# Optimization experiments

Hardware: AMD Instinct MI355X
Metric: run time of the kernel (lower is better)

Reference implementation:

```python
import jax, jax.numpy as jnp
import numpy as np

B, SQ, SKV = 4, 2048, 2048
DQ, DKV, H, NH = 1024, 1024, 1024, 16
HD = H // NH


def setup_inputs() -> dict:
    key = jax.random.key(0)
    ks = jax.random.split(key, 10)
    s = 0.02
    return {
        "query": jax.random.normal(ks[0], (B, SQ, DQ), jnp.float32),
        "key_value": jax.random.normal(ks[1], (B, SKV, DKV), jnp.float32),
        "Wq": jax.random.normal(ks[2], (DQ, H), jnp.float32) * s,
        "bq": jnp.zeros((H,), jnp.float32),
        "Wk": jax.random.normal(ks[3], (DKV, H), jnp.float32) * s,
        "bk": jnp.zeros((H,), jnp.float32),
        "Wv": jax.random.normal(ks[4], (DKV, H), jnp.float32) * s,
        "bv": jnp.zeros((H,), jnp.float32),
        "Wo": jax.random.normal(ks[5], (H, DQ), jnp.float32) * s,
        "bo": jnp.zeros((DQ,), jnp.float32),
    }


def reference(query, key_value, Wq, bq, Wk, bk, Wv, bv, Wo, bo):
    b, sq, _ = query.shape
    skv = key_value.shape[1]
    scale = np.sqrt(HD).astype(np.float32)
    # project and split heads: [B, S, H] -> [B, NH, S, HD]
    q = (query @ Wq + bq).reshape(b, sq, NH, HD).transpose(0, 2, 1, 3)
    k = (key_value @ Wk + bk).reshape(b, skv, NH, HD).transpose(0, 2, 1, 3)
    v = (key_value @ Wv + bv).reshape(b, skv, NH, HD).transpose(0, 2, 1, 3)
    scores = jnp.einsum("bhqd,bhkd->bhqk", q, k) / scale
    attn = jax.nn.softmax(scores, axis=-1)
    out = jnp.einsum("bhqk,bhkd->bhqd", attn, v)
    out = out.transpose(0, 2, 1, 3).reshape(b, sq, NH * HD)
    return out @ Wo + bo
```

## Files before the change

kernel.cpp:

```cpp
#include <hip/hip_runtime.h>


typedef short s16x8 __attribute__((ext_vector_type(8)));
typedef short s16x4 __attribute__((ext_vector_type(4)));
typedef float f32x4 __attribute__((ext_vector_type(4)));
typedef float f32x16 __attribute__((ext_vector_type(16)));
typedef unsigned short u16;
typedef unsigned int u32;

__device__ __forceinline__ u16 f2bf(float f){
    union{float f;u32 u;} v; v.f=f;
    u32 r = v.u + 0x7fffu + ((v.u>>16)&1u);
    return (u16)(r>>16);
}
__device__ __forceinline__ int swz(int row,int colB){ return row*128 + (colB ^ ((row&7)<<4)); }

__device__ __forceinline__ void gl16(const void* g, void* l){
    __builtin_amdgcn_global_load_lds((__attribute__((address_space(1))) void*)(void*)g,
                                     (__attribute__((address_space(3))) void*)l, 16, 0, 0);
}
__device__ __forceinline__ u32 cvtpk(float lo, float hi){
    u32 r; asm("v_cvt_pk_bf16_f32 %0, %1, %2" : "=v"(r) : "v"(lo), "v"(hi)); return r;
}
__device__ __forceinline__ void plswap(u32& a, u32& b){
    asm("v_permlane32_swap_b32 %0, %1" : "+v"(a), "+v"(b));
}

#define QSCALE 0.1803368801111204f

__device__ __forceinline__ void transW_body(const float* __restrict__ W, u16* __restrict__ Wt,
                                            int n0, int k0){
    __shared__ u16 T[64*68];
    const int tid = threadIdx.x;
    const int tr = tid>>4, tc = (tid&15)*4;
    #pragma unroll
    for (int p=0;p<4;++p){
        int k = p*16 + tr;
        f32x4 v = *(const f32x4*)(W + (size_t)(k0+k)*1024 + n0 + tc);
        s16x4 o;
        #pragma unroll
        for (int j=0;j<4;++j) o[j]=(short)f2bf(v[j]);
        *(s16x4*)(T + k*68 + tc) = o;
    }
    __syncthreads();
    #pragma unroll
    for (int p=0;p<4;++p){
        int n = p*16 + tr;
        s16x4 o;
        #pragma unroll
        for (int e=0;e<4;++e) o[e] = (short)T[(tc+e)*68 + n];
        *(s16x4*)(Wt + (size_t)(n0+n)*1024 + k0 + tc) = o;
    }
}

__global__ __launch_bounds__(256)
void prep(const float* __restrict__ q, const float* __restrict__ kv,
          u16* __restrict__ qbf, u16* __restrict__ kvbf,
          const float* __restrict__ W0, const float* __restrict__ W1,
          const float* __restrict__ W2, const float* __restrict__ W3,
          u16* __restrict__ T0, u16* __restrict__ T1,
          u16* __restrict__ T2, u16* __restrict__ T3)
{
    int blk = blockIdx.x;
    if (blk < 8192){
        const float* in = q; u16* out = qbf;
        if (blk >= 4096){ in = kv; out = kvbf; blk -= 4096; }
        size_t i = ((size_t)blk*256 + threadIdx.x)*8;
        f32x4 x = *(const f32x4*)(in+i), y = *(const f32x4*)(in+i+4);
        s16x8 o;
        #pragma unroll
        for (int j=0;j<4;++j){ o[j]=(short)f2bf(x[j]); o[4+j]=(short)f2bf(y[j]); }
        *(s16x8*)(out+i) = o;
    } else {
        blk -= 8192;
        int w = blk>>8, rem = blk&255;
        const float* W = (w==0)?W0:(w==1)?W1:(w==2)?W2:W3;
        u16*      Wt  = (w==0)?T0:(w==1)?T1:(w==2)?T2:T3;
        transW_body(W, Wt, (rem&15)*64, (rem>>4)*64);
    }
}

__global__ __launch_bounds__(256)
void gemm_qkv(const u16* __restrict__ qbf, const u16* __restrict__ kvbf,
              const u16* __restrict__ Wt3,
              const float* __restrict__ bq, const float* __restrict__ bk,
              const float* __restrict__ bv,
              u16* __restrict__ Qb, u16* __restrict__ Kb, u16* __restrict__ Vtb)
{
    __shared__ __align__(16) u16 As[2][128*64];
    __shared__ __align__(16) u16 Bs[2][128*64];
    const int K = 1024, N = 1024;
    const int tid = threadIdx.x, lane = tid&63, wave = tid>>6;
    const int ln = lane&15, g = lane>>4;
    const int wm = wave>>1, wn = wave&1;
    const int bm = blockIdx.x;
    const int proj = blockIdx.y >> 3, bn = blockIdx.y & 7;

    const u16* A    = proj ? kvbf : qbf;
    const u16* Bt   = Wt3 + (size_t)proj*(1024*1024);
    const float* bias = (proj==0) ? bq : (proj==1 ? bk : bv);
    const float scale = (proj==0) ? QSCALE : 1.0f;

    f32x4 acc[4][4] = {};

    const int r0g = tid>>3, cc8 = (tid&7)*8;
    const u16* aA = A  + (size_t)(bm*128 + r0g)*K + cc8;
    const u16* aB = Bt + (size_t)(bn*128 + r0g)*K + cc8;

    auto stage = [&](int k0, int buf){
        char* pa = (char*)As[buf] + tid*16;
        char* pb = (char*)Bs[buf] + tid*16;
        #pragma unroll
        for (int i=0;i<4;++i){
            gl16(aA + k0 + i*32*K, pa + i*4096);
            gl16(aB + k0 + i*32*K, pb + i*4096);
        }
    };

    stage(0, 0);
    int cur = 0;
    for (int k0=0; k0<K; k0+=64){
        if (k0+64 < K){
            stage(k0+64, cur^1);
            asm volatile("s_waitcnt vmcnt(8)" ::: "memory");
        } else {
            asm volatile("s_waitcnt vmcnt(0)" ::: "memory");
        }
        __builtin_amdgcn_s_barrier();
        #pragma unroll
        for (int kk=0;kk<2;++kk){
            s16x8 af[4], bf[4];
            #pragma unroll
            for (int mi=0;mi<4;++mi)
                af[mi] = *(const s16x8*)((const char*)As[cur] + (size_t)(wm*64+mi*16+ln)*128 + kk*64 + g*16);
            #pragma unroll
            for (int ni=0;ni<4;++ni)
                bf[ni] = *(const s16x8*)((const char*)Bs[cur] + (size_t)(wn*64+ni*16+ln)*128 + kk*64 + g*16);
            #pragma unroll
            for (int mi=0;mi<4;++mi)
                #pragma unroll
                for (int ni=0;ni<4;++ni)
                    acc[mi][ni] = __builtin_amdgcn_mfma_f32_16x16x32_bf16(af[mi], bf[ni], acc[mi][ni], 0,0,0);
        }
        __builtin_amdgcn_s_barrier();
        cur ^= 1;
    }

    if (proj == 2){
        u16* T = (u16*)As;
        #pragma unroll
        for (int mi=0;mi<4;++mi){
            #pragma unroll
            for (int ni=0;ni<4;++ni){
                int colp = wn*64 + ni*16 + ln;
                int row0 = wm*64 + mi*16 + 4*g;
                float bvv = bias[bn*128 + colp];
                s16x4 pk4;
                #pragma unroll
                for (int r=0;r<4;++r) pk4[r] = (short)f2bf(acc[mi][ni][r] + bvv);
                *(s16x4*)((char*)T + colp*256 + ((row0*2) ^ ((colp&7)<<4))) = pk4;
            }
        }
        __syncthreads();
        const int cold = tid>>1, chunk = (tid&1)*64;
        const int b = bm>>4, sbase = (bm*128)&2047;
        u16* dst = Vtb + ((size_t)(b*1024 + bn*128 + cold))*2048 + sbase + chunk;
        #pragma unroll
        for (int i=0;i<8;++i){
            s16x8 vv = *(const s16x8*)((char*)T + cold*256 + (((chunk + i*8)*2) ^ ((cold&7)<<4)));
            *(s16x8*)(dst + i*8) = vv;
        }
    } else {
        u16* C = proj ? Kb : Qb;
        #pragma unroll
        for (int mi=0;mi<4;++mi){
            #pragma unroll
            for (int ni=0;ni<4;++ni){
                int col = bn*128 + wn*64 + ni*16 + ln;
                float bvv = bias[col];
                #pragma unroll
                for (int r=0;r<4;++r){
                    int row = bm*128 + wm*64 + mi*16 + 4*g + r;
                    C[(size_t)row*N + col] = f2bf((acc[mi][ni][r] + bvv) * scale);
                }
            }
        }
    }
}

__global__ __launch_bounds__(256)
void gemm_out(const u16* __restrict__ A, const u16* __restrict__ Bt,
              const float* __restrict__ bias, float* __restrict__ C,
              int M, int N, int K)
{
    __shared__ __align__(16) u16 As[2][128*64];
    __shared__ __align__(16) u16 Bs[2][128*64];
    const int tid = threadIdx.x, lane = tid&63, wave = tid>>6;
    const int ln = lane&15, g = lane>>4;
    const int wm = wave>>1, wn = wave&1;
    const int bm = blockIdx.x, bn = blockIdx.y;

    f32x4 acc[4][4] = {};

    const int r0g = tid>>3, cc8 = (tid&7)*8;
    const u16* aA = A  + (size_t)(bm*128 + r0g)*K + cc8;
    const u16* aB = Bt + (size_t)(bn*128 + r0g)*K + cc8;

    auto stage = [&](int k0, int buf){
        char* pa = (char*)As[buf] + tid*16;
        char* pb = (char*)Bs[buf] + tid*16;
        #pragma unroll
        for (int i=0;i<4;++i){
            gl16(aA + k0 + i*32*K, pa + i*4096);
            gl16(aB + k0 + i*32*K, pb + i*4096);
        }
    };

    stage(0, 0);
    int cur = 0;
    for (int k0=0; k0<K; k0+=64){
        if (k0+64 < K){
            stage(k0+64, cur^1);
            asm volatile("s_waitcnt vmcnt(8)" ::: "memory");
        } else {
            asm volatile("s_waitcnt vmcnt(0)" ::: "memory");
        }
        __builtin_amdgcn_s_barrier();
        #pragma unroll
        for (int kk=0;kk<2;++kk){
            s16x8 af[4], bf[4];
            #pragma unroll
            for (int mi=0;mi<4;++mi)
                af[mi] = *(const s16x8*)((const char*)As[cur] + (size_t)(wm*64+mi*16+ln)*128 + kk*64 + g*16);
            #pragma unroll
            for (int ni=0;ni<4;++ni)
                bf[ni] = *(const s16x8*)((const char*)Bs[cur] + (size_t)(wn*64+ni*16+ln)*128 + kk*64 + g*16);
            #pragma unroll
            for (int mi=0;mi<4;++mi)
                #pragma unroll
                for (int ni=0;ni<4;++ni)
                    acc[mi][ni] = __builtin_amdgcn_mfma_f32_16x16x32_bf16(af[mi], bf[ni], acc[mi][ni], 0,0,0);
        }
        __builtin_amdgcn_s_barrier();
        cur ^= 1;
    }

    #pragma unroll
    for (int mi=0;mi<4;++mi){
        #pragma unroll
        for (int ni=0;ni<4;++ni){
            int col = bn*128 + wn*64 + ni*16 + ln;
            float bv = bias[col];
            #pragma unroll
            for (int r=0;r<4;++r){
                int row = bm*128 + wm*64 + mi*16 + 4*g + r;
                C[(size_t)row*N + col] = acc[mi][ni][r] + bv;
            }
        }
    }
}

__global__ __launch_bounds__(256)
void attn_fwd13(const u16* __restrict__ Q, const u16* __restrict__ K,
                const u16* __restrict__ Vt, u16* __restrict__ O)
{
    __shared__ __align__(16) char smem[32768];
    const int tid = threadIdx.x, lane = tid&63, wave = tid>>6;
    const int l31 = lane&31, hl = lane>>5;

    int dlin = blockIdx.y*16 + blockIdx.x;
    int xc = dlin&7, t0 = dlin>>3;
    int bh = xc*8 + (t0>>4), qt = t0&15;
    int b = bh>>4, h = bh&15;

    const int qrow = qt*128 + wave*32 + l31;
    const size_t qgoff = ((size_t)(b*2048 + qrow))*1024 + h*64;
    const u16* Kg = K  + ((size_t)(b*2048))*1024 + h*64;
    const u16* Vg = Vt + ((size_t)(b*1024 + h*64))*2048;

    s16x8 bq[4];
    #pragma unroll
    for (int ks=0;ks<4;++ks)
        bq[ks] = *(const s16x8*)(Q + qgoff + 16*ks + 8*hl);

    float lacc[8] = {};
    f32x16 oa0 = {}, oa1 = {};

    const int r0 = tid>>3;
    const int qc = (tid&7) ^ (r0&7);
    const u16* kbase = Kg + (size_t)r0*1024 + qc*8;
    const u16* vbase = Vg + (size_t)r0*2048 + qc*8;
    const int ldst = tid*16;

    auto stage = [&](int kt, int buf){
        char* Kb = smem + buf*16384;
        char* Vb = Kb + 8192;
        const size_t kkOff = (size_t)kt*65536;
        const int kv0 = kt*64;
        gl16(kbase + kkOff,           Kb + ldst);
        gl16(kbase + kkOff + 32768,   Kb + 4096 + ldst);
        gl16(vbase + kv0,             Vb + ldst);
        gl16(vbase + kv0 + 65536,     Vb + 4096 + ldst);
    };

    int kofs[8];
    #pragma unroll
    for (int hk=0;hk<2;++hk)
        #pragma unroll
        for (int ks=0;ks<4;++ks)
            kofs[hk*4+ks] = swz(hk*32 + l31, 32*ks + 16*hl);

    auto qk = [&](int buf, f32x16& sA, f32x16& sB){
        char* Kb = smem + buf*16384;
        f32x16 a = {}, c = {};
        __builtin_amdgcn_s_setprio(1);
        #pragma unroll
        for (int ks=0; ks<4; ++ks){
            s16x8 ak0 = *(const s16x8*)(Kb + kofs[ks]);
            s16x8 ak1 = *(const s16x8*)(Kb + kofs[4+ks]);
            a = __builtin_amdgcn_mfma_f32_32x32x16_bf16(ak0, bq[ks], a, 0,0,0);
            c = __builtin_amdgcn_mfma_f32_32x32x16_bf16(ak1, bq[ks], c, 0,0,0);
        }
        __builtin_amdgcn_s_setprio(0);
        sA = a; sB = c;
    };

    auto smpack = [&](f32x16& s0, f32x16& s1, s16x8* bP){
        #pragma unroll
        for (int r=0; r<16; ++r){
            s0[r] = __builtin_amdgcn_exp2f(s0[r]);
            s1[r] = __builtin_amdgcn_exp2f(s1[r]);
        }
        #pragma unroll
        for (int i=0;i<8;++i)
            lacc[i] += (s0[i]+s0[i+8]) + (s1[i]+s1[i+8]);
        #pragma unroll
        for (int f=0; f<2; ++f){
            const f32x16& sf = f ? s1 : s0;
            u32 W[8];
            #pragma unroll
            for (int w=0; w<8; ++w) W[w] = cvtpk(sf[2*w], sf[2*w+1]);
            #pragma unroll
            for (int s=0; s<2; ++s){
                u32 x0 = W[4*s+0], y0 = W[4*s+2];
                u32 x1 = W[4*s+1], y1 = W[4*s+3];
                plswap(x0, y0);
                plswap(x1, y1);
                union { u32 w[4]; s16x8 v; } u;
                u.w[0]=x0; u.w[1]=x1; u.w[2]=y0; u.w[3]=y1;
                bP[2*f+s] = u.v;
            }
        }
    };

    auto pv = [&](int buf, const s16x8* bP){
        char* Vb = smem + buf*16384 + 8192;
        __builtin_amdgcn_s_setprio(1);
        #pragma unroll
        for (int ks=0; ks<4; ++ks){
            s16x8 av0 = *(const s16x8*)(Vb + kofs[ks]);
            s16x8 av1 = *(const s16x8*)(Vb + kofs[4+ks]);
            oa0 = __builtin_amdgcn_mfma_f32_32x32x16_bf16(av0, bP[ks], oa0, 0,0,0);
            oa1 = __builtin_amdgcn_mfma_f32_32x32x16_bf16(av1, bP[ks], oa1, 0,0,0);
        }
        __builtin_amdgcn_s_setprio(0);
    };

    int cur = 0;
    auto body = [&](f32x16& sC0, f32x16& sC1, f32x16& sN0, f32x16& sN1, int kt){
        asm volatile("s_waitcnt vmcnt(2)" ::: "memory");
        __builtin_amdgcn_s_barrier();
        qk(cur^1, sN0, sN1);
        s16x8 bP[4];
        smpack(sC0, sC1, bP);
        pv(cur, bP);
        __builtin_amdgcn_s_barrier();
        if (kt < 30) stage(kt+2, cur);
        cur ^= 1;
    };

    stage(0, 0);
    stage(1, 1);
    asm volatile("s_waitcnt vmcnt(6)" ::: "memory");
    __builtin_amdgcn_s_barrier();
    f32x16 sa, sb, sc, sd;
    qk(0, sa, sb);

    int kt = 0;
    #pragma unroll 1
    for (int it=0; it<15; ++it){
        body(sa, sb, sc, sd, kt); ++kt;
        body(sc, sd, sa, sb, kt); ++kt;
    }
    body(sa, sb, sc, sd, kt); ++kt;

    asm volatile("s_waitcnt vmcnt(0)" ::: "memory");
    __builtin_amdgcn_s_barrier();
    {
        s16x8 bP[4];
        smpack(sc, sd, bP);
        pv(cur, bP);
    }

    float rs = ((lacc[0]+lacc[1])+(lacc[2]+lacc[3])) + ((lacc[4]+lacc[5])+(lacc[6]+lacc[7]));
    rs += __shfl_xor(rs, 32);
    float inv = 1.0f / rs;

    u16* Ob = O + qgoff;
    #pragma unroll
    for (int fd=0; fd<2; ++fd){
        const f32x16& oaf = fd ? oa1 : oa0;
        #pragma unroll
        for (int rq=0; rq<4; ++rq){
            s16x4 o;
            #pragma unroll
            for (int e=0;e<4;++e) o[e] = (short)f2bf(oaf[rq*4+e] * inv);
            *(s16x4*)(Ob + fd*32 + rq*8 + hl*4) = o;
        }
    }
}

template<bool A_IS_F32, int EPI>
__global__ __launch_bounds__(256)
void gemm_bias_64(const void* __restrict__ Av, const float* __restrict__ W,
                  const float* __restrict__ bias, void* __restrict__ Cout,
                  int M, int N, int K, float scale)
{
    __shared__ __align__(16) char smem[16384];
    char* As = smem;
    char* Ws = smem + 8192;
    const int tid  = threadIdx.x;
    const int lane = tid & 63, wave = tid >> 6;
    const int g = lane >> 4, ln = lane & 15;
    const int wm = wave >> 1, wn = wave & 1;
    const int bm = blockIdx.x, bn = blockIdx.y;
    f32x4 acc[2][2] = {};
    const int srow = tid >> 2;
    const int sch  = (tid & 3) * 16;

    for (int k0 = 0; k0 < K; k0 += 64) {
        if constexpr (A_IS_F32) {
            const float* a = (const float*)Av + (size_t)(bm*64+srow)*K + k0 + sch;
            const f32x4* a4 = (const f32x4*)a;
            #pragma unroll
            for (int c = 0; c < 2; ++c) {
                f32x4 x = a4[c*2+0], y = a4[c*2+1];
                s16x8 wv;
                #pragma unroll
                for (int j = 0; j < 4; ++j){ wv[j]=(short)f2bf(x[j]); wv[4+j]=(short)f2bf(y[j]); }
                *(s16x8*)(As + swz(srow, sch*2 + c*16)) = wv;
            }
        } else {
            const u16* a = (const u16*)Av + (size_t)(bm*64+srow)*K + k0 + sch;
            *(s16x8*)(As + swz(srow, sch*2 + 0))  = *(const s16x8*)(a + 0);
            *(s16x8*)(As + swz(srow, sch*2 + 16)) = *(const s16x8*)(a + 8);
        }
        {
            const float* wsrc = W + (size_t)(k0+srow)*N + bn*64 + sch;
            #pragma unroll
            for (int j = 0; j < 16; ++j) {
                int n = sch + j;
                *(short*)(Ws + n*128 + ((srow*2) ^ ((n&7)<<4))) = (short)f2bf(wsrc[j]);
            }
        }
        __syncthreads();
        #pragma unroll
        for (int kk = 0; kk < 2; ++kk) {
            s16x8 af[2], bfr[2];
            #pragma unroll
            for (int mi = 0; mi < 2; ++mi)
                af[mi] = *(const s16x8*)(As + swz(wm*32+mi*16+ln, kk*64 + g*16));
            #pragma unroll
            for (int ni = 0; ni < 2; ++ni)
                bfr[ni] = *(const s16x8*)(Ws + swz(wn*32+ni*16+ln, kk*64 + g*16));
            #pragma unroll
            for (int mi = 0; mi < 2; ++mi)
                #pragma unroll
                for (int ni = 0; ni < 2; ++ni)
                    acc[mi][ni] = __builtin_amdgcn_mfma_f32_16x16x32_bf16(af[mi], bfr[ni], acc[mi][ni], 0,0,0);
        }
        __syncthreads();
    }
    #pragma unroll
    for (int mi = 0; mi < 2; ++mi){
        #pragma unroll
        for (int ni = 0; ni < 2; ++ni){
            int col = bn*64 + wn*32 + ni*16 + ln;
            float bv = bias[col];
            #pragma unroll
            for (int r = 0; r < 4; ++r){
                int row = bm*64 + wm*32 + mi*16 + 4*g + r;
                float v = (acc[mi][ni][r] + bv) * scale;
                if constexpr (EPI==0)
                    ((u16*)Cout)[(size_t)row*N + col] = f2bf(v);
                else if constexpr (EPI==2){
                    int b = row>>11, s = row&2047;
                    ((u16*)Cout)[((size_t)(b*1024+col))*2048 + s] = f2bf(v);
                } else
                    ((float*)Cout)[(size_t)row*N + col] = v;
            }
        }
    }
}

extern "C" void kernel_launch(void* const* d_in, const int* in_sizes, int n_in,
                              void* d_out, int out_size, void* d_ws, size_t ws_size,
                              hipStream_t stream)
{
    const float* query = (const float*)d_in[0];
    const float* kvin  = (const float*)d_in[1];
    const float* Wq = (const float*)d_in[2];
    const float* bq = (const float*)d_in[3];
    const float* Wk = (const float*)d_in[4];
    const float* bk = (const float*)d_in[5];
    const float* Wv = (const float*)d_in[6];
    const float* bv = (const float*)d_in[7];
    const float* Wo = (const float*)d_in[8];
    const float* bo = (const float*)d_in[9];

    const int M = 8192, D = 1024;
    const size_t MB = 1024ull*1024ull;
    u16* Qb  = (u16*)d_ws;
    u16* Kb  = Qb  + 8*MB;
    u16* Vtb = Kb  + 8*MB;
    u16* Ob  = Vtb + 8*MB;

    if (ws_size >= 66*MB) {
        u16* Wt3 = Ob;
        u16* Wto = Ob + 8*MB;
        u16* qbf  = (u16*)d_out;
        u16* kvbf = qbf + 8*MB;

        prep<<<9216,256,0,stream>>>(query, kvin, qbf, kvbf,
                                    Wq, Wk, Wv, Wo,
                                    Wt3, Wt3 + 1*MB, Wt3 + 2*MB, Wto);

        gemm_qkv<<<dim3(64,24),256,0,stream>>>(qbf, kvbf, Wt3, bq, bk, bv,
                                               Qb, Kb, Vtb);

        attn_fwd13<<<dim3(16,64),256,0,stream>>>(Qb, Kb, Vtb, Ob);

        gemm_out<<<dim3(64,8),256,0,stream>>>(Ob, Wto, bo, (float*)d_out, M, D, D);
    } else {
        dim3 gg(128,16);
        gemm_bias_64<true ,0><<<gg,256,0,stream>>>(query, Wq, bq, Qb,  M, D, D, QSCALE);
        gemm_bias_64<true ,0><<<gg,256,0,stream>>>(kvin,  Wk, bk, Kb,  M, D, D, 1.0f);
        gemm_bias_64<true ,2><<<gg,256,0,stream>>>(kvin,  Wv, bv, Vtb, M, D, D, 1.0f);
        attn_fwd13<<<dim3(16,64),256,0,stream>>>(Qb, Kb, Vtb, Ob);
        gemm_bias_64<false,3><<<gg,256,0,stream>>>(Ob, Wo, bo, d_out, M, D, D, 1.0f);
    }
}
```

Baseline: 216.7 us.

## Fuse Q projection into attention kernel and drop Q from QKV GEMM

The Q projection leaves the batched QKV GEMM, which now computes only K and V. Each attention block instead computes its own 128×64 Q tile with MFMA from bf16 query rows and transposed Wq loaded straight from global memory, then adds bias, scales and packs it into the B-operand layout. This removes the Q write and re-read and one third of the projection GEMM grid, and the first K/V tiles are staged before the Q compute to overlap that latency. In exchange, Q-projection loads bypass LDS, so each wave fetches the same Wq slice redundantly with strided global loads, which adds latency and L2 traffic at the start of attention.

```diff
diff --git a/kernel.cpp b/kernel.cpp
--- a/kernel.cpp
+++ b/kernel.cpp
@@ -81,11 +81,9 @@
 }
 
 __global__ __launch_bounds__(256)
-void gemm_qkv(const u16* __restrict__ qbf, const u16* __restrict__ kvbf,
-              const u16* __restrict__ Wt3,
-              const float* __restrict__ bq, const float* __restrict__ bk,
-              const float* __restrict__ bv,
-              u16* __restrict__ Qb, u16* __restrict__ Kb, u16* __restrict__ Vtb)
+void gemm_kv(const u16* __restrict__ kvbf, const u16* __restrict__ WtKV,
+             const float* __restrict__ bk, const float* __restrict__ bv,
+             u16* __restrict__ Kb, u16* __restrict__ Vtb)
 {
     __shared__ __align__(16) u16 As[2][128*64];
     __shared__ __align__(16) u16 Bs[2][128*64];
@@ -96,16 +94,14 @@
     const int bm = blockIdx.x;
     const int proj = blockIdx.y >> 3, bn = blockIdx.y & 7;
 
-    const u16* A    = proj ? kvbf : qbf;
-    const u16* Bt   = Wt3 + (size_t)proj*(1024*1024);
-    const float* bias = (proj==0) ? bq : (proj==1 ? bk : bv);
-    const float scale = (proj==0) ? QSCALE : 1.0f;
+    const u16* Bt   = WtKV + (size_t)proj*(1024*1024);
+    const float* bias = proj ? bv : bk;
 
     f32x4 acc[4][4] = {};
 
     const int r0g = tid>>3, cc8 = (tid&7)*8;
-    const u16* aA = A  + (size_t)(bm*128 + r0g)*K + cc8;
-    const u16* aB = Bt + (size_t)(bn*128 + r0g)*K + cc8;
+    const u16* aA = kvbf + (size_t)(bm*128 + r0g)*K + cc8;
+    const u16* aB = Bt   + (size_t)(bn*128 + r0g)*K + cc8;
 
     auto stage = [&](int k0, int buf){
         char* pa = (char*)As[buf] + tid*16;
@@ -146,7 +142,7 @@
         cur ^= 1;
     }
 
-    if (proj == 2){
+    if (proj == 1){
         u16* T = (u16*)As;
         #pragma unroll
         for (int mi=0;mi<4;++mi){
@@ -171,7 +167,6 @@
             *(s16x8*)(dst + i*8) = vv;
         }
     } else {
-        u16* C = proj ? Kb : Qb;
         #pragma unroll
         for (int mi=0;mi<4;++mi){
             #pragma unroll
@@ -181,7 +176,7 @@
                 #pragma unroll
                 for (int r=0;r<4;++r){
                     int row = bm*128 + wm*64 + mi*16 + 4*g + r;
-                    C[(size_t)row*N + col] = f2bf((acc[mi][ni][r] + bvv) * scale);
+                    Kb[(size_t)row*N + col] = f2bf(acc[mi][ni][r] + bvv);
                 }
             }
         }
@@ -261,8 +256,10 @@
 }
 
 __global__ __launch_bounds__(256)
-void attn_fwd13(const u16* __restrict__ Q, const u16* __restrict__ K,
-                const u16* __restrict__ Vt, u16* __restrict__ O)
+void attn_fwd14(const u16* __restrict__ qbf, const u16* __restrict__ Wtq,
+                const float* __restrict__ biasq,
+                const u16* __restrict__ K, const u16* __restrict__ Vt,
+                u16* __restrict__ O)
 {
     __shared__ __align__(16) char smem[32768];
     const int tid = threadIdx.x, lane = tid&63, wave = tid>>6;
@@ -277,14 +274,6 @@
     const size_t qgoff = ((size_t)(b*2048 + qrow))*1024 + h*64;
     const u16* Kg = K  + ((size_t)(b*2048))*1024 + h*64;
     const u16* Vg = Vt + ((size_t)(b*1024 + h*64))*2048;
-
-    s16x8 bq[4];
-    #pragma unroll
-    for (int ks=0;ks<4;++ks)
-        bq[ks] = *(const s16x8*)(Q + qgoff + 16*ks + 8*hl);
-
-    float lacc[8] = {};
-    f32x16 oa0 = {}, oa1 = {};
 
     const int r0 = tid>>3;
     const int qc = (tid&7) ^ (r0&7);
@@ -303,6 +292,48 @@
         gl16(vbase + kv0 + 65536,     Vb + 4096 + ldst);
     };
 
+    stage(0, 0);
+    stage(1, 1);
+
+    const u16* wqp = Wtq + (size_t)(h*64 + l31)*1024 + 8*hl;
+    const u16* qap = qbf + (size_t)(b*2048 + qrow)*1024 + 8*hl;
+    f32x16 aq0 = {}, aq1 = {};
+    #pragma unroll 4
+    for (int kq=0; kq<1024; kq+=16){
+        s16x8 aw0 = *(const s16x8*)(wqp + kq);
+        s16x8 aw1 = *(const s16x8*)(wqp + 32*1024 + kq);
+        s16x8 qv  = *(const s16x8*)(qap + kq);
+        aq0 = __builtin_amdgcn_mfma_f32_32x32x16_bf16(aw0, qv, aq0, 0,0,0);
+        aq1 = __builtin_amdgcn_mfma_f32_32x32x16_bf16(aw1, qv, aq1, 0,0,0);
+    }
+    #pragma unroll
+    for (int r=0; r<16; ++r){
+        int d = (r&3) + 8*(r>>2) + 4*hl;
+        aq0[r] = (aq0[r] + biasq[h*64 + d     ]) * QSCALE;
+        aq1[r] = (aq1[r] + biasq[h*64 + 32 + d]) * QSCALE;
+    }
+    s16x8 bq[4];
+    #pragma unroll
+    for (int f=0; f<2; ++f){
+        const f32x16& sf = f ? aq1 : aq0;
+        u32 W[8];
+        #pragma unroll
+        for (int w=0; w<8; ++w) W[w] = cvtpk(sf[2*w], sf[2*w+1]);
+        #pragma unroll
+        for (int s=0; s<2; ++s){
+            u32 x0 = W[4*s+0], y0 = W[4*s+2];
+            u32 x1 = W[4*s+1], y1 = W[4*s+3];
+            plswap(x0, y0);
+            plswap(x1, y1);
+            union { u32 w[4]; s16x8 v; } u;
+            u.w[0]=x0; u.w[1]=x1; u.w[2]=y0; u.w[3]=y1;
+            bq[2*f+s] = u.v;
+        }
+    }
+
+    float lacc[8] = {};
+    f32x16 oa0 = {}, oa1 = {};
+
     int kofs[8];
     #pragma unroll
     for (int hk=0;hk<2;++hk)
@@ -364,6 +395,160 @@
             oa1 = __builtin_amdgcn_mfma_f32_32x32x16_bf16(av1, bP[ks], oa1, 0,0,0);
         }
         __builtin_amdgcn_s_setprio(0);
+    };
+
+    int cur = 0;
+    auto body = [&](f32x16& sC0, f32x16& sC1, f32x16& sN0, f32x16& sN1, int kt){
+        asm volatile("s_waitcnt vmcnt(2)" ::: "memory");
+        __builtin_amdgcn_s_barrier();
+        qk(cur^1, sN0, sN1);
+        s16x8 bP[4];
+        smpack(sC0, sC1, bP);
+        pv(cur, bP);
+        __builtin_amdgcn_s_barrier();
+        if (kt < 30) stage(kt+2, cur);
+        cur ^= 1;
+    };
+
+    asm volatile("s_waitcnt vmcnt(0)" ::: "memory");
+    __builtin_amdgcn_s_barrier();
+    f32x16 sa, sb, sc, sd;
+    qk(0, sa, sb);
+
+    int kt = 0;
+    #pragma unroll 1
+    for (int it=0; it<15; ++it){
+        body(sa, sb, sc, sd, kt); ++kt;
+        body(sc, sd, sa, sb, kt); ++kt;
+    }
+    body(sa, sb, sc, sd, kt); ++kt;
+
+    asm volatile("s_waitcnt vmcnt(0)" ::: "memory");
+    __builtin_amdgcn_s_barrier();
+    {
+        s16x8 bP[4];
+        smpack(sc, sd, bP);
+        pv(cur, bP);
+    }
+
+    float rs = ((lacc[0]+lacc[1])+(lacc[2]+lacc[3])) + ((lacc[4]+lacc[5])+(lacc[6]+lacc[7]));
+    rs += __shfl_xor(rs, 32);
+    float inv = 1.0f / rs;
+
+    u16* Ob = O + qgoff;
+    #pragma unroll
+    for (int fd=0; fd<2; ++fd){
+        const f32x16& oaf = fd ? oa1 : oa0;
+        #pragma unroll
+        for (int rq=0; rq<4; ++rq){
+            s16x4 o;
+            #pragma unroll
+            for (int e=0;e<4;++e) o[e] = (short)f2bf(oaf[rq*4+e] * inv);
+            *(s16x4*)(Ob + fd*32 + rq*8 + hl*4) = o;
+        }
+    }
+}
+
+__global__ __launch_bounds__(256)
+void attn_fwd13(const u16* __restrict__ Q, const u16* __restrict__ K,
+                const u16* __restrict__ Vt, u16* __restrict__ O)
+{
+    __shared__ __align__(16) char smem[32768];
+    const int tid = threadIdx.x, lane = tid&63, wave = tid>>6;
+    const int l31 = lane&31, hl = lane>>5;
+
+    int dlin = blockIdx.y*16 + blockIdx.x;
+    int xc = dlin&7, t0 = dlin>>3;
+    int bh = xc*8 + (t0>>4), qt = t0&15;
+    int b = bh>>4, h = bh&15;
+
+    const int qrow = qt*128 + wave*32 + l31;
+    const size_t qgoff = ((size_t)(b*2048 + qrow))*1024 + h*64;
+    const u16* Kg = K  + ((size_t)(b*2048))*1024 + h*64;
+    const u16* Vg = Vt + ((size_t)(b*1024 + h*64))*2048;
+
+    s16x8 bq[4];
+    #pragma unroll
+    for (int ks=0;ks<4;++ks)
+        bq[ks] = *(const s16x8*)(Q + qgoff + 16*ks + 8*hl);
+
+    float lacc[8] = {};
+    f32x16 oa0 = {}, oa1 = {};
+
+    const int r0 = tid>>3;
+    const int qc = (tid&7) ^ (r0&7);
+    const u16* kbase = Kg + (size_t)r0*1024 + qc*8;
+    const u16* vbase = Vg + (size_t)r0*2048 + qc*8;
+    const int ldst = tid*16;
+
+    auto stage = [&](int kt, int buf){
+        char* Kb = smem + buf*16384;
+        char* Vb = Kb + 8192;
+        const size_t kkOff = (size_t)kt*65536;
+        const int kv0 = kt*64;
+        gl16(kbase + kkOff,           Kb + ldst);
+        gl16(kbase + kkOff + 32768,   Kb + 4096 + ldst);
+        gl16(vbase + kv0,             Vb + ldst);
+        gl16(vbase + kv0 + 65536,     Vb + 4096 + ldst);
+    };
+
+    int kofs[8];
+    #pragma unroll
+    for (int hk=0;hk<2;++hk)
+        #pragma unroll
+        for (int ks=0;ks<4;++ks)
+            kofs[hk*4+ks] = swz(hk*32 + l31, 32*ks + 16*hl);
+
+    auto qk = [&](int buf, f32x16& sA, f32x16& sB){
+        char* Kb = smem + buf*16384;
+        f32x16 a = {}, c = {};
+        #pragma unroll
+        for (int ks=0; ks<4; ++ks){
+            s16x8 ak0 = *(const s16x8*)(Kb + kofs[ks]);
+            s16x8 ak1 = *(const s16x8*)(Kb + kofs[4+ks]);
+            a = __builtin_amdgcn_mfma_f32_32x32x16_bf16(ak0, bq[ks], a, 0,0,0);
+            c = __builtin_amdgcn_mfma_f32_32x32x16_bf16(ak1, bq[ks], c, 0,0,0);
+        }
+        sA = a; sB = c;
+    };
+
+    auto smpack = [&](f32x16& s0, f32x16& s1, s16x8* bP){
+        #pragma unroll
+        for (int r=0; r<16; ++r){
+            s0[r] = __builtin_amdgcn_exp2f(s0[r]);
+            s1[r] = __builtin_amdgcn_exp2f(s1[r]);
+        }
+        #pragma unroll
+        for (int i=0;i<8;++i)
+            lacc[i] += (s0[i]+s0[i+8]) + (s1[i]+s1[i+8]);
+        #pragma unroll
+        for (int f=0; f<2; ++f){
+            const f32x16& sf = f ? s1 : s0;
+            u32 W[8];
+            #pragma unroll
+            for (int w=0; w<8; ++w) W[w] = cvtpk(sf[2*w], sf[2*w+1]);
+            #pragma unroll
+            for (int s=0; s<2; ++s){
+                u32 x0 = W[4*s+0], y0 = W[4*s+2];
+                u32 x1 = W[4*s+1], y1 = W[4*s+3];
+                plswap(x0, y0);
+                plswap(x1, y1);
+                union { u32 w[4]; s16x8 v; } u;
+                u.w[0]=x0; u.w[1]=x1; u.w[2]=y0; u.w[3]=y1;
+                bP[2*f+s] = u.v;
+            }
+        }
+    };
+
+    auto pv = [&](int buf, const s16x8* bP){
+        char* Vb = smem + buf*16384 + 8192;
+        #pragma unroll
+        for (int ks=0; ks<4; ++ks){
+            s16x8 av0 = *(const s16x8*)(Vb + kofs[ks]);
+            s16x8 av1 = *(const s16x8*)(Vb + kofs[4+ks]);
+            oa0 = __builtin_amdgcn_mfma_f32_32x32x16_bf16(av0, bP[ks], oa0, 0,0,0);
+            oa1 = __builtin_amdgcn_mfma_f32_32x32x16_bf16(av1, bP[ks], oa1, 0,0,0);
+        }
     };
 
     int cur = 0;
@@ -526,19 +711,19 @@
     u16* Ob  = Vtb + 8*MB;
 
     if (ws_size >= 66*MB) {
-        u16* Wt3 = Ob;
-        u16* Wto = Ob + 8*MB;
+        u16* Wtq  = Qb;
+        u16* WtKV = Ob;
+        u16* Wto  = Ob + 8*MB;
         u16* qbf  = (u16*)d_out;
         u16* kvbf = qbf + 8*MB;
 
         prep<<<9216,256,0,stream>>>(query, kvin, qbf, kvbf,
                                     Wq, Wk, Wv, Wo,
-                                    Wt3, Wt3 + 1*MB, Wt3 + 2*MB, Wto);
-
-        gemm_qkv<<<dim3(64,24),256,0,stream>>>(qbf, kvbf, Wt3, bq, bk, bv,
-                                               Qb, Kb, Vtb);
-
-        attn_fwd13<<<dim3(16,64),256,0,stream>>>(Qb, Kb, Vtb, Ob);
+                                    Wtq, WtKV, WtKV + 1*MB, Wto);
+
+        gemm_kv<<<dim3(64,16),256,0,stream>>>(kvbf, WtKV, bk, bv, Kb, Vtb);
+
+        attn_fwd14<<<dim3(16,64),256,0,stream>>>(qbf, Wtq, bq, Kb, Vtb, Ob);
 
         gemm_out<<<dim3(64,8),256,0,stream>>>(Ob, Wto, bo, (float*)d_out, M, D, D);
     } else {
```

Result: slower. 271.3 us (+25.2%).
